# Optimization experiments

Hardware: AMD Instinct MI355X
Metric: run time of the kernel (lower is better)

The kernel has to match this reference:

```python
import jax, jax.numpy as jnp
import numpy as np

N, M, C = 32768, 8192, 128
K = 3            # number of interpolation neighbors (PointNet++/RepSurf FP)
EPS_BN = 1e-5    # torch BatchNorm1d default eps
EPS_D = 1e-8     # RepSurf dist_recip eps


def setup_inputs() -> dict:
    key = jax.random.key(0)
    ks = jax.random.split(key, 16)
    s = 0.05
    inp = {
        "pos1": jax.random.normal(ks[0], (N, 3), jnp.float32),
        "pos2": jax.random.normal(ks[1], (M, 3), jnp.float32),
        "feat2": jax.random.normal(ks[2], (M, C), jnp.float32),
    }
    # MLP stack [128,128,128]: Linear + BatchNorm1d (gamma/beta) per layer
    for i in range(3):
        inp[f"W{i}"] = jax.random.normal(ks[3 + i], (C, C), jnp.float32) * s
        inp[f"b{i}"] = jnp.zeros((C,), jnp.float32)
        inp[f"g{i}"] = jnp.ones((C,), jnp.float32)
        inp[f"be{i}"] = jnp.zeros((C,), jnp.float32)
    return inp


def _lin_bn_relu(x, W, b, g, be):
    # Linear -> BatchNorm1d (training-mode batch stats, biased var) -> ReLU
    y = x @ W.T + b
    m = y.mean(axis=0)
    v = y.var(axis=0)
    return jax.nn.relu((y - m) * jax.lax.rsqrt(v + EPS_BN) * g + be)


def reference(pos1, pos2, feat2, W0, b0, g0, be0, W1, b1, g1, be1, W2, b2, g2, be2):
    # squared pairwise distances [N, M] (memory-bound: 1 GB fp32)
    d = ((pos1 ** 2).sum(-1, keepdims=True)
         + (pos2 ** 2).sum(-1)[None, :]
         - 2.0 * (pos1 @ pos2.T))
    neg_d, idx = jax.lax.top_k(-d, K)          # 3 nearest neighbors
    dk = jnp.maximum(-neg_d, 0.0)              # [N, K] squared dists
    w = 1.0 / (dk + EPS_D)
    w = w / w.sum(-1, keepdims=True)           # inverse-distance weights
    # gather neighbor features and interpolate: [N, K, C] -> [N, C]
    interp = jnp.einsum('nkc,nk->nc', feat2[idx], w)
    x = _lin_bn_relu(interp, W0, b0, g0, be0)
    x = _lin_bn_relu(x, W1, b1, g1, be1)
    x = _lin_bn_relu(x, W2, b2, g2, be2)
    return x
```

## Files before the change

### kernel.cpp

```cpp
#include <hip/hip_runtime.h>
#include <math.h>

#define NQ 32768
#define MC 8192
#define CC 128
#define EPS_BN 1e-5f
#define EPS_D  1e-8

#define DBL_BIG 1e300
#define IDX_BIG 0x7fffffff

#define QB  64
#define TB  512
#define NW  8
#define CH  2048
#define HM  (MC / 2)
#define NCH (HM / CH)
#define SLC (CH / NW)
#define KMASK 0xFFFFE000u
#define IMASK 0x1FFFu
#define NSURV 64
#define KNN_B ((NQ / QB) * 2)
#define GEMM_B (NQ / 64)

typedef __attribute__((ext_vector_type(8))) short bf16x8;
typedef __attribute__((ext_vector_type(4))) float floatx4;
typedef unsigned short ushort_t;

__device__ __forceinline__ unsigned umin_(unsigned a, unsigned b) { return a < b ? a : b; }
__device__ __forceinline__ unsigned umax_(unsigned a, unsigned b) { return a > b ? a : b; }

__device__ __forceinline__ unsigned bf16pair(float a, float b) {
    unsigned ua = __float_as_uint(a); ua = (ua + 0x7FFFu + ((ua >> 16) & 1u)) >> 16;
    unsigned ub = __float_as_uint(b); ub = (ub + 0x7FFFu + ((ub >> 16) & 1u)) >> 16;
    return ua | (ub << 16);
}

__global__ __launch_bounds__(TB) void knn_kernel(const float* __restrict__ pos1,
                                                 const float* __restrict__ pos2,
                                                 unsigned* __restrict__ skeys,
                                                 const float* __restrict__ W0,
                                                 const float* __restrict__ W1,
                                                 const float* __restrict__ W2,
                                                 ushort_t* __restrict__ Wbf) {
    __shared__ __align__(16) float4 sp4[CH];
    __shared__ unsigned skey[QB][NW * 4];

    if (blockIdx.x >= KNN_B) {
        const int pb = blockIdx.x - KNN_B;
        const int f = pb * TB + threadIdx.x;
        const float* Ws[3] = {W0, W1, W2};
#pragma unroll
        for (int l = 0; l < 3; ++l) {
            const float4 v = ((const float4*)Ws[l])[f];
            unsigned* dst = (unsigned*)(Wbf + (size_t)l * CC * CC);
            dst[f * 2 + 0] = bf16pair(v.x, v.y);
            dst[f * 2 + 1] = bf16pair(v.z, v.w);
        }
        return;
    }

    const int half = blockIdx.x & 1;
    const int bq   = blockIdx.x >> 1;
    const int wv = threadIdx.x >> 6;
    const int ln = threadIdx.x & 63;
    const int q  = bq * QB + ln;

    const float px = pos1[q * 3 + 0];
    const float py = pos1[q * 3 + 1];
    const float pz = pos1[q * 3 + 2];
    const float s1 = px * px + py * py + pz * pz;
    const float m2x = -2.f * px, m2y = -2.f * py, m2z = -2.f * pz;

    unsigned k0 = 0xFFFFFFFFu, k1 = 0xFFFFFFFFu, k2 = 0xFFFFFFFFu, k3 = 0xFFFFFFFFu;

    for (int c0 = 0; c0 < NCH; ++c0) {
        const int cb = half * HM + c0 * CH;
        __syncthreads();
        {
            const float4* g = (const float4*)(pos2 + (size_t)(cb + threadIdx.x * 4) * 3);
            const float4 f0 = g[0], f1 = g[1], f2 = g[2];
            sp4[threadIdx.x * 4 + 0] = make_float4(f0.x, f0.y, f0.z,
                fmaf(f0.x, f0.x, fmaf(f0.y, f0.y, f0.z * f0.z)));
            sp4[threadIdx.x * 4 + 1] = make_float4(f0.w, f1.x, f1.y,
                fmaf(f0.w, f0.w, fmaf(f1.x, f1.x, f1.y * f1.y)));
            sp4[threadIdx.x * 4 + 2] = make_float4(f1.z, f1.w, f2.x,
                fmaf(f1.z, f1.z, fmaf(f1.w, f1.w, f2.x * f2.x)));
            sp4[threadIdx.x * 4 + 3] = make_float4(f2.y, f2.z, f2.w,
                fmaf(f2.y, f2.y, fmaf(f2.z, f2.z, f2.w * f2.w)));
        }
        __syncthreads();
        const float4* b4 = sp4 + wv * SLC;
        const int jb = cb + wv * SLC;
#pragma unroll 4
        for (int e = 0; e < SLC; ++e) {
            const float4 c = b4[e];
            const float d = fmaf(m2x, c.x, fmaf(m2y, c.y, fmaf(m2z, c.z, c.w + s1)));
            unsigned ek = (__float_as_uint(d) & KMASK) | (unsigned)(jb + e);
            if (ek < k3) {
                unsigned t;
                t = umin_(k0, ek); ek = umax_(k0, ek); k0 = t;
                t = umin_(k1, ek); ek = umax_(k1, ek); k1 = t;
                t = umin_(k2, ek); ek = umax_(k2, ek); k2 = t;
                k3 = umin_(k3, ek);
            }
        }
    }
    skey[ln][wv * 4 + 0] = k0;
    skey[ln][wv * 4 + 1] = k1;
    skey[ln][wv * 4 + 2] = k2;
    skey[ln][wv * 4 + 3] = k3;
    __syncthreads();

#pragma unroll
    for (int t = threadIdx.x * 4; t < threadIdx.x * 4 + 4; ++t) {
        const int ql = t >> 5, slot = t & 31;
        skeys[(size_t)(bq * QB + ql) * NSURV + half * 32 + slot] = skey[ql][slot];
    }
}

template <int MODE>
__global__ __launch_bounds__(256) void gemm_mfma(const float* __restrict__ Xsrc,
                                                 const unsigned* __restrict__ skeys,
                                                 const float* __restrict__ pos1,
                                                 const float* __restrict__ pos2,
                                                 const float* __restrict__ scaleIn,
                                                 const float* __restrict__ shiftIn,
                                                 const ushort_t* __restrict__ Wb,
                                                 const float* __restrict__ bias,
                                                 float* __restrict__ Y,
                                                 float* __restrict__ partials) {
    __shared__ __align__(16) short xa[64][136];
    __shared__ __align__(16) short wb[128][136];
    __shared__ float blk_s[CC], blk_q[CC];

    const int row0 = blockIdx.x * 64;

    if constexpr (MODE == 0) {
        __shared__ int   lidx[QB][3];
        __shared__ float lw[QB][3];
        {
            double* rrd = (double*)&xa[0][0];
            int*    rri = (int*)&wb[0][0];
            const int ql = threadIdx.x >> 2;
            const int pp = threadIdx.x & 3;
            const int qg = row0 + ql;
            const double qx = (double)pos1[qg * 3 + 0];
            const double qy = (double)pos1[qg * 3 + 1];
            const double qz = (double)pos1[qg * 3 + 2];
            double b0 = DBL_BIG, b1 = DBL_BIG, b2 = DBL_BIG;
            int    j0 = IDX_BIG, j1 = IDX_BIG, j2 = IDX_BIG;
            const uint4* kp = (const uint4*)(skeys + (size_t)qg * NSURV + pp * 16);
#pragma unroll
            for (int gi = 0; gi < 4; ++gi) {
                const uint4 kk = kp[gi];
                const unsigned ks[4] = {kk.x, kk.y, kk.z, kk.w};
#pragma unroll
                for (int u = 0; u < 4; ++u) {
                    const int id = (int)(ks[u] & IMASK);
                    const double x = (double)pos2[id * 3 + 0];
                    const double y = (double)pos2[id * 3 + 1];
                    const double z = (double)pos2[id * 3 + 2];
                    const double ax = qx - x, ay = qy - y, az = qz - z;
                    const double d = ax * ax + ay * ay + az * az;
                    const bool l2 = (d < b2) || (d == b2 && id < j2);
                    if (l2) {
                        const bool l1 = (d < b1) || (d == b1 && id < j1);
                        const bool l0 = (d < b0) || (d == b0 && id < j0);
                        b2 = l1 ? b1 : d;              j2 = l1 ? j1 : id;
                        b1 = l1 ? (l0 ? b0 : d) : b1;  j1 = l1 ? (l0 ? j0 : id) : j1;
                        b0 = l0 ? d : b0;              j0 = l0 ? id : j0;
                    }
                }
            }
            const int base = (ql * 4 + pp) * 3;
            rrd[base + 0] = b0; rri[base + 0] = j0;
            rrd[base + 1] = b1; rri[base + 1] = j1;
            rrd[base + 2] = b2; rri[base + 2] = j2;
            __syncthreads();
            if (threadIdx.x < QB) {
                const int qq = threadIdx.x;
                double c0 = DBL_BIG, c1 = DBL_BIG, c2 = DBL_BIG;
                int    i0 = IDX_BIG, i1 = IDX_BIG, i2 = IDX_BIG;
#pragma unroll
                for (int s = 0; s < 12; ++s) {
                    const double d = rrd[qq * 12 + s];
                    const int   id = rri[qq * 12 + s];
                    const bool l2 = (d < c2) || (d == c2 && id < i2);
                    if (l2) {
                        const bool l1 = (d < c1) || (d == c1 && id < i1);
                        const bool l0 = (d < c0) || (d == c0 && id < i0);
                        c2 = l1 ? c1 : d;              i2 = l1 ? i1 : id;
                        c1 = l1 ? (l0 ? c0 : d) : c1;  i1 = l1 ? (l0 ? i0 : id) : i1;
                        c0 = l0 ? d : c0;              i0 = l0 ? id : i0;
                    }
                }
                const double r0 = 1.0 / (c0 + EPS_D);
                const double r1 = 1.0 / (c1 + EPS_D);
                const double r2 = 1.0 / (c2 + EPS_D);
                const double inv = 1.0 / (r0 + r1 + r2);
                lidx[qq][0] = i0; lidx[qq][1] = i1; lidx[qq][2] = i2;
                lw[qq][0] = (float)(r0 * inv);
                lw[qq][1] = (float)(r1 * inv);
                lw[qq][2] = (float)(r2 * inv);
            }
            __syncthreads();
        }
        if (threadIdx.x < CC) { blk_s[threadIdx.x] = 0.f; blk_q[threadIdx.x] = 0.f; }
#pragma unroll
        for (int e = threadIdx.x; e < 64 * 32; e += 256) {
            const int r = e >> 5, c4 = e & 31;
            const int i0 = lidx[r][0], i1 = lidx[r][1], i2 = lidx[r][2];
            const float w0 = lw[r][0], w1 = lw[r][1], w2 = lw[r][2];
            const float4 f0 = *(const float4*)&Xsrc[(size_t)i0 * CC + c4 * 4];
            const float4 f1 = *(const float4*)&Xsrc[(size_t)i1 * CC + c4 * 4];
            const float4 f2 = *(const float4*)&Xsrc[(size_t)i2 * CC + c4 * 4];
            float4 v;
            v.x = w0 * f0.x + w1 * f1.x + w2 * f2.x;
            v.y = w0 * f0.y + w1 * f1.y + w2 * f2.y;
            v.z = w0 * f0.z + w1 * f1.z + w2 * f2.z;
            v.w = w0 * f0.w + w1 * f1.w + w2 * f2.w;
            unsigned* dst = (unsigned*)&xa[r][0];
            dst[c4 * 2 + 0] = bf16pair(v.x, v.y);
            dst[c4 * 2 + 1] = bf16pair(v.z, v.w);
        }
    } else {
        if (threadIdx.x < CC) { blk_s[threadIdx.x] = 0.f; blk_q[threadIdx.x] = 0.f; }
#pragma unroll
        for (int e = threadIdx.x; e < 64 * 32; e += 256) {
            const int r = e >> 5, c4 = e & 31;
            const float4 x  = *(const float4*)&Xsrc[(size_t)(row0 + r) * CC + c4 * 4];
            const float4 sc = *(const float4*)&scaleIn[c4 * 4];
            const float4 sh = *(const float4*)&shiftIn[c4 * 4];
            float4 v;
            v.x = fmaxf(fmaf(x.x, sc.x, sh.x), 0.f);
            v.y = fmaxf(fmaf(x.y, sc.y, sh.y), 0.f);
            v.z = fmaxf(fmaf(x.z, sc.z, sh.z), 0.f);
            v.w = fmaxf(fmaf(x.w, sc.w, sh.w), 0.f);
            unsigned* dst = (unsigned*)&xa[r][0];
            dst[c4 * 2 + 0] = bf16pair(v.x, v.y);
            dst[c4 * 2 + 1] = bf16pair(v.z, v.w);
        }
    }
#pragma unroll
    for (int e = threadIdx.x; e < 128 * 16; e += 256) {
        const int co = e >> 4, seg = e & 15;
        *(float4*)&wb[co][seg * 8] = *(const float4*)&Wb[(size_t)co * CC + seg * 8];
    }
    __syncthreads();

    const int lane = threadIdx.x & 63;
    const int wv = threadIdx.x >> 6;
    const int nn = lane & 15;
    const int quad = lane >> 4;

    floatx4 acc[8] = {};

    const short* arow = &xa[wv * 16 + nn][0];
#pragma unroll
    for (int ks = 0; ks < 4; ++ks) {
        const bf16x8 a = *(const bf16x8*)(arow + ks * 32 + quad * 8);
#pragma unroll
        for (int ct = 0; ct < 8; ++ct) {
            const bf16x8 b = *(const bf16x8*)(&wb[ct * 16 + nn][0] + ks * 32 + quad * 8);
            acc[ct] = __builtin_amdgcn_mfma_f32_16x16x32_bf16(a, b, acc[ct], 0, 0, 0);
        }
    }

#pragma unroll
    for (int ct = 0; ct < 8; ++ct) {
        const float bv = bias[ct * 16 + nn];
        float s = 0.f, qv = 0.f;
#pragma unroll
        for (int r = 0; r < 4; ++r) {
            acc[ct][r] += bv;
            s += acc[ct][r];
            qv = fmaf(acc[ct][r], acc[ct][r], qv);
        }
#pragma unroll
        for (int r = 0; r < 4; ++r)
            Y[(size_t)(row0 + wv * 16 + quad * 4 + r) * CC + ct * 16 + nn] = acc[ct][r];
        s += __shfl_xor(s, 16, 64); s += __shfl_xor(s, 32, 64);
        qv += __shfl_xor(qv, 16, 64); qv += __shfl_xor(qv, 32, 64);
        if (quad == 0) {
            atomicAdd(&blk_s[ct * 16 + nn], s);
            atomicAdd(&blk_q[ct * 16 + nn], qv);
        }
    }
    __syncthreads();
    {
        const int ch = threadIdx.x;
        const float v = (ch < CC) ? blk_s[ch] : blk_q[ch - CC];
        partials[(size_t)ch * GEMM_B + blockIdx.x] = v;
    }
}

__global__ __launch_bounds__(256) void reduce_stats(const float* __restrict__ P,
                                                    const float* __restrict__ g,
                                                    const float* __restrict__ be,
                                                    float* __restrict__ sc,
                                                    float* __restrict__ sh) {
    __shared__ float accS[4], accQ[4];
    const int c = blockIdx.x;
    const int t = threadIdx.x;
    float s  = P[(size_t)c * GEMM_B + t]        + P[(size_t)c * GEMM_B + 256 + t];
    float qv = P[(size_t)(c + CC) * GEMM_B + t] + P[(size_t)(c + CC) * GEMM_B + 256 + t];
#pragma unroll
    for (int off = 32; off >= 1; off >>= 1) {
        s  += __shfl_xor(s, off, 64);
        qv += __shfl_xor(qv, off, 64);
    }
    if ((t & 63) == 0) { accS[t >> 6] = s; accQ[t >> 6] = qv; }
    __syncthreads();
    if (t == 0) {
        const float S = accS[0] + accS[1] + accS[2] + accS[3];
        const float Q = accQ[0] + accQ[1] + accQ[2] + accQ[3];
        const float m = S * (1.f / (float)NQ);
        const float v = fmaf(-m, m, Q * (1.f / (float)NQ));
        const float rstd = rsqrtf(v + EPS_BN);
        const float scl = g[c] * rstd;
        sc[c] = scl;
        sh[c] = fmaf(-m, scl, be[c]);
    }
}

__global__ __launch_bounds__(256) void bn_relu_kernel(const float* __restrict__ Y,
                                                      const float* __restrict__ sc,
                                                      const float* __restrict__ sh,
                                                      float* __restrict__ out) {
    const int i4 = blockIdx.x * 256 + threadIdx.x;
    const int c4 = (i4 & 31) * 4;
    const float4 y = ((const float4*)Y)[i4];
    const float4 s = *(const float4*)&sc[c4];
    const float4 h = *(const float4*)&sh[c4];
    float4 o;
    o.x = fmaxf(fmaf(y.x, s.x, h.x), 0.f);
    o.y = fmaxf(fmaf(y.y, s.y, h.y), 0.f);
    o.z = fmaxf(fmaf(y.z, s.z, h.z), 0.f);
    o.w = fmaxf(fmaf(y.w, s.w, h.w), 0.f);
    ((float4*)out)[i4] = o;
}

extern "C" void kernel_launch(void* const* d_in, const int* in_sizes, int n_in,
                              void* d_out, int out_size, void* d_ws, size_t ws_size,
                              hipStream_t stream) {
    (void)in_sizes; (void)n_in; (void)out_size; (void)ws_size;

    const float* pos1  = (const float*)d_in[0];
    const float* pos2  = (const float*)d_in[1];
    const float* feat2 = (const float*)d_in[2];
    const float* Wl[3]  = {(const float*)d_in[3], (const float*)d_in[7],  (const float*)d_in[11]};
    const float* bl[3]  = {(const float*)d_in[4], (const float*)d_in[8],  (const float*)d_in[12]};
    const float* gl[3]  = {(const float*)d_in[5], (const float*)d_in[9],  (const float*)d_in[13]};
    const float* bel[3] = {(const float*)d_in[6], (const float*)d_in[10], (const float*)d_in[14]};

    float* ws = (float*)d_ws;
    float* B0   = ws;
    float* B1   = B0 + (size_t)NQ * CC;
    unsigned* skeys = (unsigned*)B1;
    float* part = B1 + (size_t)NQ * CC;
    float* scsh = part + 256 * GEMM_B;
    ushort_t* Wbf = (ushort_t*)(scsh + 3 * 256);

    float* sc0 = scsh + 0 * 256; float* sh0 = sc0 + CC;
    float* sc1 = scsh + 1 * 256; float* sh1 = sc1 + CC;
    float* sc2 = scsh + 2 * 256; float* sh2 = sc2 + CC;

    knn_kernel<<<KNN_B + 8, TB, 0, stream>>>(pos1, pos2, skeys,
                                             Wl[0], Wl[1], Wl[2], Wbf);
    gemm_mfma<0><<<GEMM_B, 256, 0, stream>>>(feat2, skeys, pos1, pos2,
                                             nullptr, nullptr,
                                             Wbf + 0 * CC * CC, bl[0], B0, part);
    reduce_stats<<<CC, 256, 0, stream>>>(part, gl[0], bel[0], sc0, sh0);
    gemm_mfma<1><<<GEMM_B, 256, 0, stream>>>(B0, nullptr, nullptr, nullptr,
                                             sc0, sh0,
                                             Wbf + 1 * CC * CC, bl[1], B1, part);
    reduce_stats<<<CC, 256, 0, stream>>>(part, gl[1], bel[1], sc1, sh1);
    gemm_mfma<1><<<GEMM_B, 256, 0, stream>>>(B1, nullptr, nullptr, nullptr,
                                             sc1, sh1,
                                             Wbf + 2 * CC * CC, bl[2], B0, part);
    reduce_stats<<<CC, 256, 0, stream>>>(part, gl[2], bel[2], sc2, sh2);
    bn_relu_kernel<<<(size_t)NQ * CC / 1024, 256, 0, stream>>>(B0, sc2, sh2, (float*)d_out);
}
```

Baseline: 230.9 us.

## Fuse BN stat reduction into GEMMs via atomics and rework KNN distance loop

Removes the three reduce_stats launches. Each GEMM now atomically adds its per-block sums into 8 grouped stat buffers, which the knn kernel zeroes up front, and the next GEMM or the final BN kernel folds them into scale and shift itself. The KNN kernel now loads raw xyz into shared memory without precomputing squared norms, computes the distance directly as a difference-squared, and drops the branch around the insertion sort. This cuts launch count and partial-buffer traffic, at the cost of atomic contention, nondeterministic summation order, and more ALU work per candidate in the KNN loop.

```diff
diff --git a/kernel.cpp b/kernel.cpp
--- a/kernel.cpp
+++ b/kernel.cpp
@@ -22,6 +22,7 @@
 #define NSURV 64
 #define KNN_B ((NQ / QB) * 2)
 #define GEMM_B (NQ / 64)
+#define NGRP 8
 
 typedef __attribute__((ext_vector_type(8))) short bf16x8;
 typedef __attribute__((ext_vector_type(4))) float floatx4;
@@ -42,8 +43,9 @@
                                                  const float* __restrict__ W0,
                                                  const float* __restrict__ W1,
                                                  const float* __restrict__ W2,
-                                                 ushort_t* __restrict__ Wbf) {
-    __shared__ __align__(16) float4 sp4[CH];
+                                                 ushort_t* __restrict__ Wbf,
+                                                 float* __restrict__ stats) {
+    __shared__ __align__(16) float4 sp4[CH * 3 / 4];
     __shared__ unsigned skey[QB][NW * 4];
 
     if (blockIdx.x >= KNN_B) {
@@ -57,6 +59,8 @@
             dst[f * 2 + 0] = bf16pair(v.x, v.y);
             dst[f * 2 + 1] = bf16pair(v.z, v.w);
         }
+        if (pb == 0)
+            for (int i = threadIdx.x; i < 3 * NGRP * 256; i += TB) stats[i] = 0.f;
         return;
     }
 
@@ -69,8 +73,6 @@
     const float px = pos1[q * 3 + 0];
     const float py = pos1[q * 3 + 1];
     const float pz = pos1[q * 3 + 2];
-    const float s1 = px * px + py * py + pz * pz;
-    const float m2x = -2.f * px, m2y = -2.f * py, m2z = -2.f * pz;
 
     unsigned k0 = 0xFFFFFFFFu, k1 = 0xFFFFFFFFu, k2 = 0xFFFFFFFFu, k3 = 0xFFFFFFFFu;
 
@@ -78,31 +80,32 @@
         const int cb = half * HM + c0 * CH;
         __syncthreads();
         {
-            const float4* g = (const float4*)(pos2 + (size_t)(cb + threadIdx.x * 4) * 3);
-            const float4 f0 = g[0], f1 = g[1], f2 = g[2];
-            sp4[threadIdx.x * 4 + 0] = make_float4(f0.x, f0.y, f0.z,
-                fmaf(f0.x, f0.x, fmaf(f0.y, f0.y, f0.z * f0.z)));
-            sp4[threadIdx.x * 4 + 1] = make_float4(f0.w, f1.x, f1.y,
-                fmaf(f0.w, f0.w, fmaf(f1.x, f1.x, f1.y * f1.y)));
-            sp4[threadIdx.x * 4 + 2] = make_float4(f1.z, f1.w, f2.x,
-                fmaf(f1.z, f1.z, fmaf(f1.w, f1.w, f2.x * f2.x)));
-            sp4[threadIdx.x * 4 + 3] = make_float4(f2.y, f2.z, f2.w,
-                fmaf(f2.y, f2.y, fmaf(f2.z, f2.z, f2.w * f2.w)));
+            const float4* g4 = (const float4*)(pos2 + (size_t)cb * 3);
+#pragma unroll
+            for (int i = threadIdx.x; i < CH * 3 / 4; i += TB) sp4[i] = g4[i];
         }
         __syncthreads();
-        const float4* b4 = sp4 + wv * SLC;
+        const float4* b4 = sp4 + wv * (SLC * 3 / 4);
         const int jb = cb + wv * SLC;
-#pragma unroll 4
-        for (int e = 0; e < SLC; ++e) {
-            const float4 c = b4[e];
-            const float d = fmaf(m2x, c.x, fmaf(m2y, c.y, fmaf(m2z, c.z, c.w + s1)));
-            unsigned ek = (__float_as_uint(d) & KMASK) | (unsigned)(jb + e);
-            if (ek < k3) {
+#pragma unroll 2
+        for (int gi = 0; gi < SLC / 4; ++gi) {
+            const float4 A = b4[gi * 3 + 0];
+            const float4 B = b4[gi * 3 + 1];
+            const float4 Cv = b4[gi * 3 + 2];
+            const int j = jb + gi * 4;
+            const float cx[4] = {A.x, A.w, B.z, Cv.y};
+            const float cy[4] = {A.y, B.x, B.w, Cv.z};
+            const float cz[4] = {A.z, B.y, Cv.x, Cv.w};
+#pragma unroll
+            for (int u = 0; u < 4; ++u) {
+                const float dx = px - cx[u], dy = py - cy[u], dz = pz - cz[u];
+                const float d = fmaf(dx, dx, fmaf(dy, dy, dz * dz));
+                unsigned e = (__float_as_uint(d) & KMASK) | (unsigned)(j + u);
                 unsigned t;
-                t = umin_(k0, ek); ek = umax_(k0, ek); k0 = t;
-                t = umin_(k1, ek); ek = umax_(k1, ek); k1 = t;
-                t = umin_(k2, ek); ek = umax_(k2, ek); k2 = t;
-                k3 = umin_(k3, ek);
+                t = umin_(k0, e); e = umax_(k0, e); k0 = t;
+                t = umin_(k1, e); e = umax_(k1, e); k1 = t;
+                t = umin_(k2, e); e = umax_(k2, e); k2 = t;
+                k3 = umin_(k3, e);
             }
         }
     }
@@ -124,15 +127,17 @@
                                                  const unsigned* __restrict__ skeys,
                                                  const float* __restrict__ pos1,
                                                  const float* __restrict__ pos2,
-                                                 const float* __restrict__ scaleIn,
-                                                 const float* __restrict__ shiftIn,
+                                                 const float* __restrict__ statsIn,
+                                                 const float* __restrict__ gIn,
+                                                 const float* __restrict__ beIn,
                                                  const ushort_t* __restrict__ Wb,
                                                  const float* __restrict__ bias,
                                                  float* __restrict__ Y,
-                                                 float* __restrict__ partials) {
+                                                 float* __restrict__ statsOut) {
     __shared__ __align__(16) short xa[64][136];
     __shared__ __align__(16) short wb[128][136];
     __shared__ float blk_s[CC], blk_q[CC];
+    __shared__ float sc_l[CC], sh_l[CC];
 
     const int row0 = blockIdx.x * 64;
 
@@ -225,13 +230,29 @@
             dst[c4 * 2 + 1] = bf16pair(v.z, v.w);
         }
     } else {
-        if (threadIdx.x < CC) { blk_s[threadIdx.x] = 0.f; blk_q[threadIdx.x] = 0.f; }
+        if (threadIdx.x < CC) {
+            const int c = threadIdx.x;
+            float s = 0.f, q = 0.f;
+#pragma unroll
+            for (int gr = 0; gr < NGRP; ++gr) {
+                s += statsIn[gr * 256 + c];
+                q += statsIn[gr * 256 + CC + c];
+            }
+            const float m = s * (1.f / (float)NQ);
+            const float v = fmaf(-m, m, q * (1.f / (float)NQ));
+            const float rstd = rsqrtf(v + EPS_BN);
+            const float scl = gIn[c] * rstd;
+            sc_l[c] = scl;
+            sh_l[c] = fmaf(-m, scl, beIn[c]);
+            blk_s[c] = 0.f; blk_q[c] = 0.f;
+        }
+        __syncthreads();
 #pragma unroll
         for (int e = threadIdx.x; e < 64 * 32; e += 256) {
             const int r = e >> 5, c4 = e & 31;
             const float4 x  = *(const float4*)&Xsrc[(size_t)(row0 + r) * CC + c4 * 4];
-            const float4 sc = *(const float4*)&scaleIn[c4 * 4];
-            const float4 sh = *(const float4*)&shiftIn[c4 * 4];
+            const float4 sc = *(const float4*)&sc_l[c4 * 4];
+            const float4 sh = *(const float4*)&sh_l[c4 * 4];
             float4 v;
             v.x = fmaxf(fmaf(x.x, sc.x, sh.x), 0.f);
             v.y = fmaxf(fmaf(x.y, sc.y, sh.y), 0.f);
@@ -291,54 +312,49 @@
     {
         const int ch = threadIdx.x;
         const float v = (ch < CC) ? blk_s[ch] : blk_q[ch - CC];
-        partials[(size_t)ch * GEMM_B + blockIdx.x] = v;
-    }
-}
-
-__global__ __launch_bounds__(256) void reduce_stats(const float* __restrict__ P,
-                                                    const float* __restrict__ g,
-                                                    const float* __restrict__ be,
-                                                    float* __restrict__ sc,
-                                                    float* __restrict__ sh) {
-    __shared__ float accS[4], accQ[4];
-    const int c = blockIdx.x;
-    const int t = threadIdx.x;
-    float s  = P[(size_t)c * GEMM_B + t]        + P[(size_t)c * GEMM_B + 256 + t];
-    float qv = P[(size_t)(c + CC) * GEMM_B + t] + P[(size_t)(c + CC) * GEMM_B + 256 + t];
-#pragma unroll
-    for (int off = 32; off >= 1; off >>= 1) {
-        s  += __shfl_xor(s, off, 64);
-        qv += __shfl_xor(qv, off, 64);
-    }
-    if ((t & 63) == 0) { accS[t >> 6] = s; accQ[t >> 6] = qv; }
-    __syncthreads();
-    if (t == 0) {
-        const float S = accS[0] + accS[1] + accS[2] + accS[3];
-        const float Q = accQ[0] + accQ[1] + accQ[2] + accQ[3];
-        const float m = S * (1.f / (float)NQ);
-        const float v = fmaf(-m, m, Q * (1.f / (float)NQ));
+        atomicAdd(&statsOut[(blockIdx.x & (NGRP - 1)) * 256 + ch], v);
+    }
+}
+
+__global__ __launch_bounds__(256) void bn_final(const float* __restrict__ Y,
+                                                const float* __restrict__ statsIn,
+                                                const float* __restrict__ g,
+                                                const float* __restrict__ be,
+                                                float* __restrict__ out) {
+    __shared__ float sc_l[CC], sh_l[CC];
+    if (threadIdx.x < CC) {
+        const int c = threadIdx.x;
+        float s = 0.f, q = 0.f;
+#pragma unroll
+        for (int gr = 0; gr < NGRP; ++gr) {
+            s += statsIn[gr * 256 + c];
+            q += statsIn[gr * 256 + CC + c];
+        }
+        const float m = s * (1.f / (float)NQ);
+        const float v = fmaf(-m, m, q * (1.f / (float)NQ));
         const float rstd = rsqrtf(v + EPS_BN);
         const float scl = g[c] * rstd;
-        sc[c] = scl;
-        sh[c] = fmaf(-m, scl, be[c]);
-    }
-}
-
-__global__ __launch_bounds__(256) void bn_relu_kernel(const float* __restrict__ Y,
-                                                      const float* __restrict__ sc,
-                                                      const float* __restrict__ sh,
-                                                      float* __restrict__ out) {
-    const int i4 = blockIdx.x * 256 + threadIdx.x;
-    const int c4 = (i4 & 31) * 4;
-    const float4 y = ((const float4*)Y)[i4];
-    const float4 s = *(const float4*)&sc[c4];
-    const float4 h = *(const float4*)&sh[c4];
-    float4 o;
-    o.x = fmaxf(fmaf(y.x, s.x, h.x), 0.f);
-    o.y = fmaxf(fmaf(y.y, s.y, h.y), 0.f);
-    o.z = fmaxf(fmaf(y.z, s.z, h.z), 0.f);
-    o.w = fmaxf(fmaf(y.w, s.w, h.w), 0.f);
-    ((float4*)out)[i4] = o;
+        sc_l[c] = scl;
+        sh_l[c] = fmaf(-m, scl, be[c]);
+    }
+    __syncthreads();
+    const float4* Y4 = (const float4*)Y;
+    float4* O4 = (float4*)out;
+    const int base = blockIdx.x * 2048 + threadIdx.x;
+#pragma unroll
+    for (int it = 0; it < 8; ++it) {
+        const int i4 = base + it * 256;
+        const int c4 = (i4 & 31) * 4;
+        const float4 y = Y4[i4];
+        const float4 s = *(const float4*)&sc_l[c4];
+        const float4 h = *(const float4*)&sh_l[c4];
+        float4 o;
+        o.x = fmaxf(fmaf(y.x, s.x, h.x), 0.f);
+        o.y = fmaxf(fmaf(y.y, s.y, h.y), 0.f);
+        o.z = fmaxf(fmaf(y.z, s.z, h.z), 0.f);
+        o.w = fmaxf(fmaf(y.w, s.w, h.w), 0.f);
+        O4[i4] = o;
+    }
 }
 
 extern "C" void kernel_launch(void* const* d_in, const int* in_sizes, int n_in,
@@ -358,27 +374,23 @@
     float* B0   = ws;
     float* B1   = B0 + (size_t)NQ * CC;
     unsigned* skeys = (unsigned*)B1;
-    float* part = B1 + (size_t)NQ * CC;
-    float* scsh = part + 256 * GEMM_B;
-    ushort_t* Wbf = (ushort_t*)(scsh + 3 * 256);
-
-    float* sc0 = scsh + 0 * 256; float* sh0 = sc0 + CC;
-    float* sc1 = scsh + 1 * 256; float* sh1 = sc1 + CC;
-    float* sc2 = scsh + 2 * 256; float* sh2 = sc2 + CC;
+    float* stats = B1 + (size_t)NQ * CC;
+    ushort_t* Wbf = (ushort_t*)(stats + 3 * NGRP * 256);
+
+    float* st0 = stats + 0 * NGRP * 256;
+    float* st1 = stats + 1 * NGRP * 256;
+    float* st2 = stats + 2 * NGRP * 256;
 
     knn_kernel<<<KNN_B + 8, TB, 0, stream>>>(pos1, pos2, skeys,
-                                             Wl[0], Wl[1], Wl[2], Wbf);
+                                             Wl[0], Wl[1], Wl[2], Wbf, stats);
     gemm_mfma<0><<<GEMM_B, 256, 0, stream>>>(feat2, skeys, pos1, pos2,
-                                             nullptr, nullptr,
-                                             Wbf + 0 * CC * CC, bl[0], B0, part);
-    reduce_stats<<<CC, 256, 0, stream>>>(part, gl[0], bel[0], sc0, sh0);
+                                             nullptr, nullptr, nullptr,
+                                             Wbf + 0 * CC * CC, bl[0], B0, st0);
     gemm_mfma<1><<<GEMM_B, 256, 0, stream>>>(B0, nullptr, nullptr, nullptr,
-                                             sc0, sh0,
-                                             Wbf + 1 * CC * CC, bl[1], B1, part);
-    reduce_stats<<<CC, 256, 0, stream>>>(part, gl[1], bel[1], sc1, sh1);
+                                             st0, gl[0], bel[0],
+                                             Wbf + 1 * CC * CC, bl[1], B1, st1);
     gemm_mfma<1><<<GEMM_B, 256, 0, stream>>>(B1, nullptr, nullptr, nullptr,
-                                             sc1, sh1,
-                                             Wbf + 2 * CC * CC, bl[2], B0, part);
-    reduce_stats<<<CC, 256, 0, stream>>>(part, gl[2], bel[2], sc2, sh2);
-    bn_relu_kernel<<<(size_t)NQ * CC / 1024, 256, 0, stream>>>(B0, sc2, sh2, (float*)d_out);
-}
+                                             st1, gl[1], bel[1],
+                                             Wbf + 2 * CC * CC, bl[2], B0, st2);
+    bn_final<<<GEMM_B, 256, 0, stream>>>(B0, st2, gl[2], bel[2], (float*)d_out);
+}
```

Result: faster. 217.4 us (-5.9%).
